# Kernel optimization log

Hardware: AMD Instinct MI355X
Metric: run time of the kernel (lower is better)

Reference implementation:

```python
import jax, jax.numpy as jnp
import numpy as np

TAU = 0.07          # temperature
NUM_CLASSES = 1000  # label vocabulary size (used for bincount length)


def setup_inputs() -> dict:
    key = jax.random.key(0)
    kq, kk, ky = jax.random.split(key, 3)
    N, K, D = 8192, 8, 512
    q = jax.random.normal(kq, (N, D), dtype=jnp.float32)
    q = q / jnp.linalg.norm(q, axis=1, keepdims=True)          # L2-normalized anchors
    k = jax.random.normal(kk, (N, K, D), dtype=jnp.float32)
    k = k / jnp.linalg.norm(k, axis=2, keepdims=True)          # L2-normalized positives
    y = jax.random.randint(ky, (N,), 0, NUM_CLASSES, dtype=jnp.int32)
    return {"q": q, "k": k, "y": y}


def reference(q, k, y):
    # q: [N, D] anchors, k: [N, K, D] external positives, y: [N] labels
    N, K, D = k.shape
    neg_inf = jnp.float32(-jnp.inf)

    # similarities to external positives and within-batch, scaled by temperature
    k_sims = jnp.einsum('nd,nkd->nk', q, k) / TAU            # [N, K]
    batch_sims = jnp.matmul(q, q.T) / TAU                    # [N, N]

    same = y[:, None] == y[None, :]                          # [N, N] label equality
    eye = jnp.eye(N, dtype=bool)
    same_class_mask = same & ~eye                            # in-batch positives (excl. self)
    same_class_counts = same_class_mask.sum(axis=1) + K      # [N]

    # faithful to torch: multiply by mask then masked_fill(x == 0, -inf)
    batch_pos = batch_sims * same_class_mask
    batch_pos = jnp.where(batch_pos == 0, neg_inf, batch_pos)
    pos_sims = jnp.concatenate([k_sims, batch_pos], axis=1)  # [N, K+N]
    num = jax.scipy.special.logsumexp(pos_sims, axis=1)      # [N]

    y_counts = jnp.bincount(y, length=NUM_CLASSES)           # [C]
    neg_sims = batch_sims * (~same)
    neg_sims = jnp.where(neg_sims == 0, neg_inf, neg_sims)
    # class-frequency-weighted denominator (as in the original, no max-shift)
    den = jnp.log(jnp.sum(jnp.exp(neg_sims) / y_counts[y][None, :].astype(q.dtype), axis=1))

    loss = -(num - den) / same_class_counts.astype(q.dtype)
    return loss.mean()
```

## Files before the change

kernel.cpp:

```cpp
#include <hip/hip_runtime.h>
#include <hip/hip_fp8.h>
#include <stdint.h>

constexpr int N    = 8192;
constexpr int D    = 512;
constexpr int KEXT = 8;
constexpr int NCLS = 1000;
#define TAU_INV  14.285714285714285714f
#define SC_L2    4.539816423767765f

typedef long   long2_t __attribute__((ext_vector_type(2)));
typedef float  f32x4   __attribute__((ext_vector_type(4)));
typedef int    v8i     __attribute__((ext_vector_type(8)));

typedef __attribute__((address_space(1))) void gvoid;
typedef __attribute__((address_space(3))) void lvoid;

__device__ __forceinline__ uint32_t pack4_e4m3(float a, float b, float c, float d) {
    __hip_fp8_e4m3 A(a), B(b), C(c), D(d);
    return (uint32_t)A.__x | ((uint32_t)B.__x << 8) |
           ((uint32_t)C.__x << 16) | ((uint32_t)D.__x << 24);
}

__device__ __forceinline__ f32x4 mfma128(long2_t alo, long2_t ahi,
                                         long2_t blo, long2_t bhi, f32x4 c) {
    union U { long2_t h[2]; v8i v; } A, B;
    A.h[0] = alo; A.h[1] = ahi;
    B.h[0] = blo; B.h[1] = bhi;
    return __builtin_amdgcn_mfma_scale_f32_16x16x128_f8f6f4(
        A.v, B.v, c, 0, 0, 0, 127, 0, 127);
}

__global__ void prep_k(const float* __restrict__ q, const int* __restrict__ y,
                       uint32_t* __restrict__ qf8, int* __restrict__ counts,
                       float* __restrict__ invy, float* __restrict__ pos,
                       float* __restrict__ neg) {
    const int b = blockIdx.x, tid = threadIdx.x;
    if (b == 0) {
        __shared__ int h[NCLS];
        for (int i = tid; i < NCLS; i += 256) h[i] = 0;
        __syncthreads();
        for (int i = tid; i < N; i += 256) atomicAdd(&h[y[i]], 1);
        __syncthreads();
        for (int i = tid; i < NCLS; i += 256) counts[i] = h[i];
        for (int i = tid; i < N; i += 256) invy[i] = 1.0f / (float)h[y[i]];
        return;
    }
    const int gid = (b - 1) * 256 + tid;
    const int row = gid >> 4;
    const int kb  = gid & 15;
    const int ks4 = kb >> 2, quad = kb & 3;
    const float* src = q + (size_t)row * D + kb * 32;
    uint32_t o[8];
#pragma unroll
    for (int j = 0; j < 8; j++) {
        float4 v = *reinterpret_cast<const float4*>(src + j * 4);
        o[j] = pack4_e4m3(v.x * SC_L2, v.y * SC_L2, v.z * SC_L2, v.w * SC_L2);
    }
    const int t = row >> 4, l15 = row & 15;
    const size_t s16 = (size_t)((t * 4 + ks4) * 128) + quad * 16 + l15;
    uint4* dst = reinterpret_cast<uint4*>(qf8);
    dst[s16]      = make_uint4(o[0], o[1], o[2], o[3]);
    dst[s16 + 64] = make_uint4(o[4], o[5], o[6], o[7]);
    if (gid < N) { pos[gid] = 0.f; neg[gid] = 0.f; }
}

__global__ __launch_bounds__(256, 2) void gemm_k(
        const uint32_t* __restrict__ qf8,
        const int* __restrict__ y,
        const float* __restrict__ invy,
        float* __restrict__ pos_sum,
        float* __restrict__ neg_sum) {
    __shared__ long2_t Asl[4096];
    __shared__ int   yR[128];
    __shared__ float redP[2][128];
    __shared__ float redN[2][128];

    const int tid  = threadIdx.x;
    const int wave = tid >> 6;
    const int lane = tid & 63;
    const int quad = lane >> 4;
    const int l15  = lane & 15;

    const int ib     = blockIdx.x >> 3;
    const int jchunk = blockIdx.x & 7;
    const int ibase  = ib * 128;

    {
        const uint32_t* src = qf8 + (size_t)ib * 16384;
#pragma unroll
        for (int it = 0; it < 16; it++) {
            const int idx = it * 256 + tid;
            __builtin_amdgcn_global_load_lds((gvoid*)(src + idx * 4),
                                             (lvoid*)(Asl + idx), 16, 0, 0);
        }
    }
    if (tid < 128) yR[tid] = y[ibase + tid];
    __syncthreads();

    const int wr = (wave >> 1) * 64;
    const int wc = (wave & 1) * 64;
    const int half = wave & 1;

    int yi[16];
#pragma unroll
    for (int mi = 0; mi < 4; mi++)
#pragma unroll
        for (int r = 0; r < 4; r++)
            yi[mi * 4 + r] = yR[wr + mi * 16 + quad * 4 + r];

    float posp[16], negp[16];
#pragma unroll
    for (int e = 0; e < 16; e++) { posp[e] = 0.f; negp[e] = 0.f; }

    const long2_t* fbL = reinterpret_cast<const long2_t*>(qf8);
    const long2_t* pB[4];
#pragma unroll
    for (int m = 0; m < 4; m++)
        pB[m] = fbL + (size_t)(jchunk * 64 + (wc >> 4) + m) * 512 + lane;

    const int tA = wr >> 4;

    for (int jt = 0; jt < 8; jt++) {
        const int j0 = jchunk * 1024 + jt * 128;

        int   yjv[4];
        float icj[4];
#pragma unroll
        for (int mj = 0; mj < 4; mj++) {
            int jc = j0 + wc + mj * 16 + l15;
            yjv[mj] = y[jc];
            icj[mj] = invy[jc];
        }

        f32x4 acc[4][4];
#pragma unroll
        for (int a = 0; a < 4; a++)
#pragma unroll
            for (int c = 0; c < 4; c++) acc[a][c] = (f32x4)0.0f;

        long2_t blo[2][4], bhi[2][4];
#pragma unroll
        for (int m = 0; m < 4; m++) {
            blo[0][m] = pB[m][0];
            bhi[0][m] = pB[m][64];
        }
#pragma unroll
        for (int ks4 = 0; ks4 < 4; ks4++) {
            const int cur = ks4 & 1, nxt = cur ^ 1;
            if (ks4 < 3) {
#pragma unroll
                for (int m = 0; m < 4; m++) {
                    blo[nxt][m] = pB[m][(ks4 + 1) * 128];
                    bhi[nxt][m] = pB[m][(ks4 + 1) * 128 + 64];
                }
            }
            long2_t alo[4], ahi[4];
#pragma unroll
            for (int m = 0; m < 4; m++) {
                alo[m] = Asl[((tA + m) * 4 + ks4) * 128 + lane];
                ahi[m] = Asl[((tA + m) * 4 + ks4) * 128 + 64 + lane];
            }
#pragma unroll
            for (int mi = 0; mi < 4; mi++)
#pragma unroll
                for (int mj = 0; mj < 4; mj++)
                    acc[mi][mj] = mfma128(alo[mi], ahi[mi],
                                          blo[cur][mj], bhi[cur][mj],
                                          acc[mi][mj]);
        }
#pragma unroll
        for (int m = 0; m < 4; m++) pB[m] += 4096;

#pragma unroll
        for (int mi = 0; mi < 4; mi++) {
#pragma unroll
            for (int r = 0; r < 4; r++) {
                const int e    = mi * 4 + r;
                const int irow = ibase + wr + mi * 16 + quad * 4 + r;
                const int myi  = yi[e];
                float ps = 0.f, ns = 0.f;
#pragma unroll
                for (int mj = 0; mj < 4; mj++) {
                    const int jcol = j0 + wc + mj * 16 + l15;
                    float a    = acc[mi][mj][r];
                    float ex   = __builtin_amdgcn_exp2f(a);
                    bool  nz   = (a != 0.0f);
                    bool  same = (myi == yjv[mj]);
                    ps += (same && (irow != jcol) && nz) ? ex : 0.0f;
                    ns += (!same && nz) ? ex * icj[mj] : 0.0f;
                }
                posp[e] += ps;
                negp[e] += ns;
            }
        }
    }

#pragma unroll
    for (int mi = 0; mi < 4; mi++) {
#pragma unroll
        for (int r = 0; r < 4; r++) {
            const int e = mi * 4 + r;
            float ps = posp[e], ns = negp[e];
#pragma unroll
            for (int off = 1; off < 16; off <<= 1) {
                ps += __shfl_xor(ps, off);
                ns += __shfl_xor(ns, off);
            }
            if (l15 == 0) {
                const int il = wr + mi * 16 + quad * 4 + r;
                redP[half][il] = ps;
                redN[half][il] = ns;
            }
        }
    }
    __syncthreads();
    if (tid < 128) {
        atomicAdd(&pos_sum[ibase + tid], redP[0][tid] + redP[1][tid]);
    } else if (tid < 256) {
        const int il = tid - 128;
        atomicAdd(&neg_sum[ibase + il], redN[0][il] + redN[1][il]);
    }
}

__global__ void finalize_k(const float* __restrict__ q, const float* __restrict__ kmat,
                           const int* __restrict__ y, const int* __restrict__ counts,
                           const float* __restrict__ pos_sum, const float* __restrict__ neg_sum,
                           float* __restrict__ loss) {
    const int wave = threadIdx.x >> 6, lane = threadIdx.x & 63;
    const int i = blockIdx.x * 4 + wave;

    const float4* q4 = reinterpret_cast<const float4*>(q) + (size_t)i * 128;
    const float4* k4 = reinterpret_cast<const float4*>(kmat) + (size_t)i * KEXT * 128;
    float4 qa = q4[lane], qb = q4[lane + 64];

    float esum = 0.f;
    for (int kk = 0; kk < KEXT; kk++) {
        float4 ka = k4[(size_t)kk * 128 + lane];
        float4 kb = k4[(size_t)kk * 128 + lane + 64];
        float p = qa.x * ka.x;
        p = fmaf(qa.y, ka.y, p); p = fmaf(qa.z, ka.z, p); p = fmaf(qa.w, ka.w, p);
        p = fmaf(qb.x, kb.x, p); p = fmaf(qb.y, kb.y, p);
        p = fmaf(qb.z, kb.z, p); p = fmaf(qb.w, kb.w, p);
#pragma unroll
        for (int off = 1; off < 64; off <<= 1) p += __shfl_xor(p, off);
        esum += __expf(p * TAU_INV);
    }
    if (lane == 0) {
        float num = logf(esum + pos_sum[i]);
        float den = logf(neg_sum[i]);
        float cnt = (float)(counts[y[i]] - 1 + KEXT);
        loss[i] = -(num - den) / cnt;
    }
}

__global__ void reduce_k(const float* __restrict__ loss, float* __restrict__ out) {
    __shared__ float part[16];
    int tid = threadIdx.x;
    float s = 0.f;
    for (int i = tid; i < N; i += 1024) s += loss[i];
#pragma unroll
    for (int off = 1; off < 64; off <<= 1) s += __shfl_xor(s, off);
    if ((tid & 63) == 0) part[tid >> 6] = s;
    __syncthreads();
    if (tid < 16) {
        float v = part[tid];
#pragma unroll
        for (int off = 1; off < 16; off <<= 1) v += __shfl_xor(v, off);
        if (tid == 0) out[0] = v / (float)N;
    }
}

extern "C" void kernel_launch(void* const* d_in, const int* in_sizes, int n_in,
                              void* d_out, int out_size, void* d_ws, size_t ws_size,
                              hipStream_t stream) {
    const float* q    = (const float*)d_in[0];
    const float* kmat = (const float*)d_in[1];
    const int*   y    = (const int*)d_in[2];
    float* out = (float*)d_out;

    char* ws = (char*)d_ws;
    uint32_t* qf8  = (uint32_t*)ws;
    int*   counts  = (int*)  (ws + 4194304);
    float* invy    = (float*)(ws + 4198400);
    float* pos     = (float*)(ws + 4231168);
    float* neg     = (float*)(ws + 4263936);
    float* loss    = (float*)(ws + 4296704);

    prep_k    <<<1 + (N * 16) / 256, 256, 0, stream>>>(q, y, qf8, counts, invy, pos, neg);
    gemm_k    <<<512, 256, 0, stream>>>(qf8, y, invy, pos, neg);
    finalize_k<<<N / 4, 256, 0, stream>>>(q, kmat, y, counts, pos, neg, loss);
    reduce_k  <<<1, 1024, 0, stream>>>(loss, out);
}
```

Baseline: 312.5 us.

## Drop B double-buffering and per-row register accumulators to cut register pressure

Removes the register double-buffer for B fragments, so each k-step now loads its B fragments directly before its MFMAs. It also replaces the 32 per-thread partial-sum registers with a shuffle reduction after every j-tile, accumulated into shared memory. The aim is to lower VGPR usage and perhaps raise occupancy. In exchange it loses load/compute overlap within a wave and adds eight times as many cross-lane shuffle reductions and LDS read-modify-writes.

```diff
diff --git a/kernel.cpp b/kernel.cpp
--- a/kernel.cpp
+++ b/kernel.cpp
@@ -95,7 +95,11 @@
                                              (lvoid*)(Asl + idx), 16, 0, 0);
         }
     }
-    if (tid < 128) yR[tid] = y[ibase + tid];
+    if (tid < 128) {
+        yR[tid] = y[ibase + tid];
+        redP[0][tid] = 0.f; redP[1][tid] = 0.f;
+        redN[0][tid] = 0.f; redN[1][tid] = 0.f;
+    }
     __syncthreads();
 
     const int wr = (wave >> 1) * 64;
@@ -108,10 +112,6 @@
 #pragma unroll
         for (int r = 0; r < 4; r++)
             yi[mi * 4 + r] = yR[wr + mi * 16 + quad * 4 + r];
-
-    float posp[16], negp[16];
-#pragma unroll
-    for (int e = 0; e < 16; e++) { posp[e] = 0.f; negp[e] = 0.f; }
 
     const long2_t* fbL = reinterpret_cast<const long2_t*>(qf8);
     const long2_t* pB[4];
@@ -139,21 +139,13 @@
 #pragma unroll
             for (int c = 0; c < 4; c++) acc[a][c] = (f32x4)0.0f;
 
-        long2_t blo[2][4], bhi[2][4];
-#pragma unroll
-        for (int m = 0; m < 4; m++) {
-            blo[0][m] = pB[m][0];
-            bhi[0][m] = pB[m][64];
-        }
 #pragma unroll
         for (int ks4 = 0; ks4 < 4; ks4++) {
-            const int cur = ks4 & 1, nxt = cur ^ 1;
-            if (ks4 < 3) {
-#pragma unroll
-                for (int m = 0; m < 4; m++) {
-                    blo[nxt][m] = pB[m][(ks4 + 1) * 128];
-                    bhi[nxt][m] = pB[m][(ks4 + 1) * 128 + 64];
-                }
+            long2_t blo[4], bhi[4];
+#pragma unroll
+            for (int m = 0; m < 4; m++) {
+                blo[m] = pB[m][ks4 * 128];
+                bhi[m] = pB[m][ks4 * 128 + 64];
             }
             long2_t alo[4], ahi[4];
 #pragma unroll
@@ -166,7 +158,7 @@
 #pragma unroll
                 for (int mj = 0; mj < 4; mj++)
                     acc[mi][mj] = mfma128(alo[mi], ahi[mi],
-                                          blo[cur][mj], bhi[cur][mj],
+                                          blo[mj], bhi[mj],
                                           acc[mi][mj]);
         }
 #pragma unroll
@@ -176,9 +168,8 @@
         for (int mi = 0; mi < 4; mi++) {
 #pragma unroll
             for (int r = 0; r < 4; r++) {
-                const int e    = mi * 4 + r;
                 const int irow = ibase + wr + mi * 16 + quad * 4 + r;
-                const int myi  = yi[e];
+                const int myi  = yi[mi * 4 + r];
                 float ps = 0.f, ns = 0.f;
 #pragma unroll
                 for (int mj = 0; mj < 4; mj++) {
@@ -190,30 +181,20 @@
                     ps += (same && (irow != jcol) && nz) ? ex : 0.0f;
                     ns += (!same && nz) ? ex * icj[mj] : 0.0f;
                 }
-                posp[e] += ps;
-                negp[e] += ns;
+#pragma unroll
+                for (int off = 1; off < 16; off <<= 1) {
+                    ps += __shfl_xor(ps, off);
+                    ns += __shfl_xor(ns, off);
+                }
+                if (l15 == 0) {
+                    const int il = wr + mi * 16 + quad * 4 + r;
+                    redP[half][il] += ps;
+                    redN[half][il] += ns;
+                }
             }
         }
     }
 
-#pragma unroll
-    for (int mi = 0; mi < 4; mi++) {
-#pragma unroll
-        for (int r = 0; r < 4; r++) {
-            const int e = mi * 4 + r;
-            float ps = posp[e], ns = negp[e];
-#pragma unroll
-            for (int off = 1; off < 16; off <<= 1) {
-                ps += __shfl_xor(ps, off);
-                ns += __shfl_xor(ns, off);
-            }
-            if (l15 == 0) {
-                const int il = wr + mi * 16 + quad * 4 + r;
-                redP[half][il] = ps;
-                redN[half][il] = ns;
-            }
-        }
-    }
     __syncthreads();
     if (tid < 128) {
         atomicAdd(&pos_sum[ibase + tid], redP[0][tid] + redP[1][tid]);
```

Measured after the change: 327.4 us. 1.05x slower.
